# Kernel optimization log

Hardware: AMD Instinct MI355X
Metric: run time of the kernel (lower is better)

## Reference

```python
import jax, jax.numpy as jnp
import numpy as np

TEMPERATURE = 1.0
NEG = -1e9
EPS = 1e-8


def setup_inputs() -> dict:
    key = jax.random.key(0)
    k1, k2, k3 = jax.random.split(key, 3)
    B, H = 524288, 32
    scores = jax.random.normal(k1, (B, H), dtype=jnp.float32)
    rankings = jax.random.randint(k2, (B, H), 0, 33, dtype=jnp.int32)
    mask = jax.random.randint(k3, (B, H), 0, 2, dtype=jnp.int32).astype(bool)
    return {"scores": scores, "rankings": rankings, "mask": mask}


def reference(scores, rankings, mask):
    B, H = scores.shape
    # effective validity: horse present AND has a ranking > 0 (top_k=None)
    m = mask & (rankings > 0)
    # masked, temperature-scaled scores; -1e9 entries underflow to exactly 0 in softmax
    s = jnp.where(m, scores / TEMPERATURE, NEG)
    p = jax.nn.softmax(s, axis=1)  # [B, H], ~0 at invalid slots

    n_valid = jnp.sum(m, axis=1)  # [B]
    # ideal order: valid horses sorted by ranking ascending (invalid pushed to end)
    rank_key = jnp.where(m, rankings, jnp.iinfo(jnp.int32).max)
    rank_order = jnp.argsort(rank_key, axis=1)          # stable sort
    # prediction order: valid horses in original index order (matches torch.where)
    pos_order = jnp.argsort(~m, axis=1)                 # stable: valid first

    q = jnp.take_along_axis(p, rank_order, axis=1)      # ideal_probs, aligned by list position
    pr = jnp.take_along_axis(p, pos_order, axis=1)      # pred_probs,  aligned by list position

    # positions >= n_valid are padding
    valid_pos = jnp.arange(H)[None, :] < n_valid[:, None]
    q_safe = jnp.where(valid_pos, q, 1.0)
    pr_safe = jnp.where(valid_pos, pr, 1.0)
    # KL(ideal || pred) with the original's log(pred + 1e-8)
    kl_terms = q_safe * (jnp.log(q_safe) - jnp.log(pr_safe + EPS))
    kl = jnp.sum(jnp.where(valid_pos, kl_terms, 0.0), axis=1)  # [B]

    # rows with <= 1 valid ranked horse are skipped entirely
    row_ok = n_valid > 1
    n_rows = jnp.maximum(jnp.sum(row_ok), 1)
    return jnp.sum(jnp.where(row_ok, kl, 0.0)) / n_rows  # reduction='mean'
```

## Files before the change

kernel.cpp:

```cpp
#include <hip/hip_runtime.h>
#include <stdint.h>


#define H 32
#define BLK 256
#define WPB 4
#define ROWD 17
#define WREGION (64 * ROWD)

__global__ __launch_bounds__(BLK) void listwise_kernel(
    const float* __restrict__ scores,
    const int* __restrict__ rankings,
    const unsigned char* __restrict__ mask_u8,
    float* __restrict__ part_kl,
    float* __restrict__ part_cnt,
    int nrows)
{
    __shared__ uint32_t stage[WPB * WREGION];
    __shared__ float s_kl[WPB], s_cnt[WPB];

    const int tid  = threadIdx.x;
    const int lane = tid & 63;
    const int wid  = tid >> 6;
    uint32_t* wbuf = &stage[wid * WREGION];
    const int wrow0 = blockIdx.x * BLK + wid * 64;

    float kl = 0.0f, cnt = 0.0f;
    uint32_t kp[16], sw[16];
    int nv = 0;
    bool have_row = false;
    unsigned short* rowp = (unsigned short*)&wbuf[lane * ROWD];

    const bool full = (wrow0 + 64 <= nrows);

    uint4 pr[8], ps[8];
    uint32_t pmw[8];
    if (full) {
        const uint4* r4 = (const uint4*)(rankings + (size_t)wrow0 * H);
        const uint4* s4 = (const uint4*)(scores + (size_t)wrow0 * H);
        const uint32_t* m1 = (const uint32_t*)(mask_u8 + (size_t)wrow0 * H);
        #pragma unroll
        for (int c = 0; c < 8; ++c) pr[c] = r4[lane + 64 * c];
        #pragma unroll
        for (int c = 0; c < 8; ++c) ps[c] = s4[lane + 64 * c];
        #pragma unroll
        for (int c = 0; c < 8; ++c) pmw[c] = m1[lane + 64 * c];
    }

    unsigned char probe = mask_u8[lane];
    const bool mask_is_i32 =
        (__ballot(((lane & 3) != 0) && (probe != 0)) == 0ull);

    if (full) {
        have_row = true;

        #pragma unroll
        for (int c = 0; c < 8; ++c) {
            const uint4 v = ps[c];
            const int L = (lane + 64 * c) << 2;
            uint32_t* d = &wbuf[(L >> 5) * ROWD + ((L & 31) >> 1)];
            d[0] = ((v.x + 0x8000u) >> 16) | (((v.y + 0x8000u) >> 16) << 16);
            d[1] = ((v.z + 0x8000u) >> 16) | (((v.w + 0x8000u) >> 16) << 16);
        }
        {
            const uint32_t* rb = &wbuf[lane * ROWD];
            #pragma unroll
            for (int a = 0; a < 16; ++a) sw[a] = rb[a];
        }

        if (!mask_is_i32) {
            #pragma unroll
            for (int c = 0; c < 8; ++c) {
                const uint4 rv = pr[c];
                const uint32_t mv = pmw[c];
                const int L = (lane + 64 * c) << 2;
                const uint32_t t0 = ((mv & 0x000000FFu) != 0u && (int)rv.x > 0) ? (rv.x << 5) : 0x4000u;
                const uint32_t t1 = ((mv & 0x0000FF00u) != 0u && (int)rv.y > 0) ? (rv.y << 5) : 0x4000u;
                const uint32_t t2 = ((mv & 0x00FF0000u) != 0u && (int)rv.z > 0) ? (rv.z << 5) : 0x4000u;
                const uint32_t t3 = ((mv & 0xFF000000u) != 0u && (int)rv.w > 0) ? (rv.w << 5) : 0x4000u;
                uint32_t* d = &wbuf[(L >> 5) * ROWD + ((L & 31) >> 1)];
                d[0] = t0 | (t1 << 16);
                d[1] = t2 | (t3 << 16);
            }
        } else {
            const uint4* m4 =
                (const uint4*)((const uint32_t*)mask_u8 + (size_t)wrow0 * H);
            #pragma unroll
            for (int c = 0; c < 8; ++c) {
                const uint4 rv = pr[c];
                const uint4 mv = m4[lane + 64 * c];
                const int L = (lane + 64 * c) << 2;
                const uint32_t t0 = (mv.x != 0u && (int)rv.x > 0) ? (rv.x << 5) : 0x4000u;
                const uint32_t t1 = (mv.y != 0u && (int)rv.y > 0) ? (rv.y << 5) : 0x4000u;
                const uint32_t t2 = (mv.z != 0u && (int)rv.z > 0) ? (rv.z << 5) : 0x4000u;
                const uint32_t t3 = (mv.w != 0u && (int)rv.w > 0) ? (rv.w << 5) : 0x4000u;
                uint32_t* d = &wbuf[(L >> 5) * ROWD + ((L & 31) >> 1)];
                d[0] = t0 | (t1 << 16);
                d[1] = t2 | (t3 << 16);
            }
        }
        {
            const uint32_t* rb = &wbuf[lane * ROWD];
            uint32_t inv2 = 0;
            #pragma unroll
            for (int a = 0; a < 16; ++a) {
                const uint32_t w = rb[a];
                kp[a] = w | ((uint32_t)(2 * a) | (((uint32_t)(2 * a + 1)) << 16));
                inv2 += (w >> 14) & 0x00010001u;
            }
            nv = 32 - (int)((inv2 & 0xFFFFu) + (inv2 >> 16));
        }
        {
            int jp = 0;
            #pragma unroll
            for (int a = 0; a < 16; ++a) {
                const uint32_t s2 = sw[a];
                const uint32_t kw = kp[a];
                const bool v0 = (kw & 0xFFFFu) < 0x4000u;
                const bool v1 = (kw >> 16) < 0x4000u;
                rowp[v0 ? jp : 33] = (unsigned short)(s2 & 0xFFFFu);
                jp += v0 ? 1 : 0;
                rowp[v1 ? jp : 33] = (unsigned short)(s2 >> 16);
                jp += v1 ? 1 : 0;
            }
        }
    } else if (wrow0 + lane < nrows) {
        have_row = true;
        const int row = wrow0 + lane;
        const int*   rptr = rankings + (size_t)row * H;
        const float* sptr = scores + (size_t)row * H;
        uint32_t vbits = 0;
        if (mask_is_i32) {
            const int* mp = (const int*)mask_u8 + (size_t)row * H;
            #pragma unroll
            for (int k = 0; k < H; ++k) vbits |= (mp[k] != 0 ? 1u : 0u) << k;
        } else {
            const unsigned char* mp = mask_u8 + (size_t)row * H;
            #pragma unroll
            for (int k = 0; k < H; ++k) vbits |= (mp[k] != 0 ? 1u : 0u) << k;
        }
        int jp = 0;
        #pragma unroll
        for (int a = 0; a < 16; ++a) {
            uint32_t kq[2], bq[2];
            #pragma unroll
            for (int q = 0; q < 2; ++q) {
                const int k = 2 * a + q;
                const int r = rptr[k];
                const bool valid = (((vbits >> k) & 1u) != 0u) && (r > 0);
                kq[q] = valid ? ((((uint32_t)r) << 5) | (uint32_t)k)
                              : (0x4000u | (uint32_t)k);
                nv += valid ? 1 : 0;
                bq[q] = (__float_as_uint(sptr[k]) + 0x8000u) >> 16;
                rowp[valid ? jp : 33] = (unsigned short)bq[q];
                jp += valid ? 1 : 0;
            }
            kp[a] = kq[0] | (kq[1] << 16);
            sw[a] = bq[0] | (bq[1] << 16);
        }
    }

    if (have_row) {
        uint32_t w32[32];
        #pragma unroll
        for (int a = 0; a < 16; ++a) {
            const uint32_t kw = kp[a], s2 = sw[a];
            w32[2 * a]     = (kw << 16) | (s2 & 0xFFFFu);
            w32[2 * a + 1] = (kw & 0xFFFF0000u) | (s2 >> 16);
        }
        #pragma unroll
        for (int k = 2; k <= 32; k <<= 1) {
            #pragma unroll
            for (int j = k >> 1; j > 0; j >>= 1) {
                #pragma unroll
                for (int i = 0; i < 32; ++i) {
                    const int l = i ^ j;
                    if (l > i) {
                        const uint32_t a = w32[i], b = w32[l];
                        const uint32_t mn = a < b ? a : b;
                        const uint32_t mx = a < b ? b : a;
                        const bool up = ((i & k) == 0);
                        w32[i] = up ? mn : mx;
                        w32[l] = up ? mx : mn;
                    }
                }
            }
        }

        float se = 0.0f, num = 0.0f;
        const uint32_t* rbd = &wbuf[lane * ROWD];
        #pragma unroll
        for (int a = 0; a < 16; ++a) {
            const uint32_t cw = rbd[a];
            #pragma unroll
            for (int q = 0; q < 2; ++q) {
                const uint32_t wv = w32[2 * a + q];
                const bool valid = wv < 0x40000000u;
                const float s_i = __uint_as_float(wv << 16);
                const uint32_t c16 = q ? (cw >> 16) : (cw & 0xFFFFu);
                const float g = __uint_as_float(c16 << 16);
                float e = __expf(s_i);
                e = valid ? e : 0.0f;
                const float d2 = valid ? (s_i - g) : 0.0f;
                se += e;
                num = __builtin_fmaf(e, d2, num);
            }
        }
        if (nv > 1) { kl = __fdividef(num, se); cnt = 1.0f; }
    }

    #pragma unroll
    for (int m = 32; m >= 1; m >>= 1) {
        kl  += __shfl_xor(kl, m);
        cnt += __shfl_xor(cnt, m);
    }
    if (lane == 0) { s_kl[wid] = kl; s_cnt[wid] = cnt; }
    __syncthreads();
    if (tid == 0) {
        part_kl[blockIdx.x]  = s_kl[0] + s_kl[1] + s_kl[2] + s_kl[3];
        part_cnt[blockIdx.x] = s_cnt[0] + s_cnt[1] + s_cnt[2] + s_cnt[3];
    }
}

__global__ __launch_bounds__(256) void finalize_kernel(
    const float* __restrict__ part_kl,
    const float* __restrict__ part_cnt,
    float* __restrict__ out, int nblk)
{
    float k = 0.0f, c = 0.0f;
    for (int i = threadIdx.x; i < nblk; i += 256) {
        k += part_kl[i];
        c += part_cnt[i];
    }
    #pragma unroll
    for (int m = 32; m >= 1; m >>= 1) {
        k += __shfl_xor(k, m);
        c += __shfl_xor(c, m);
    }
    __shared__ float sk[4], sc[4];
    const int wid = threadIdx.x >> 6;
    if ((threadIdx.x & 63) == 0) { sk[wid] = k; sc[wid] = c; }
    __syncthreads();
    if (threadIdx.x == 0) {
        float K = sk[0] + sk[1] + sk[2] + sk[3];
        float C = sc[0] + sc[1] + sc[2] + sc[3];
        if (C < 1.0f) C = 1.0f;
        out[0] = K / C;
    }
}

extern "C" void kernel_launch(void* const* d_in, const int* in_sizes, int n_in,
                              void* d_out, int out_size, void* d_ws, size_t ws_size,
                              hipStream_t stream) {
    const float* scores = (const float*)d_in[0];
    const int* rankings = (const int*)d_in[1];
    const unsigned char* mask = (const unsigned char*)d_in[2];
    float* out = (float*)d_out;

    const int total = in_sizes[0];
    const int nrows = total / H;
    const int blocks = (nrows + BLK - 1) / BLK;

    float* part_kl  = (float*)d_ws;
    float* part_cnt = (float*)d_ws + blocks;

    listwise_kernel<<<blocks, BLK, 0, stream>>>(
        scores, rankings, mask, part_kl, part_cnt, nrows);

    finalize_kernel<<<1, 256, 0, stream>>>(part_kl, part_cnt, out, blocks);
}
```

Measured before the change: 199.7 us.

## Replace LDS compaction with second bitonic sort for prediction order

Rather than compacting valid scores through LDS with scattered 16-bit stores, the kernel builds a second key array (validity and column index packed with the score) and sorts it with a bitonic network in registers, which yields the prediction order. The staging layout changes to one packed 32-bit word per element, written with uint4 stores and row stride 36. n_valid>1 is now tested on the second sorted element. This removes the serial compaction pass and scattered LDS traffic but doubles the sorting ALU work and raises register pressure, with a launch-bounds hint of 4.

```diff
diff --git a/kernel.cpp b/kernel.cpp
--- a/kernel.cpp
+++ b/kernel.cpp
@@ -5,10 +5,31 @@
 #define H 32
 #define BLK 256
 #define WPB 4
-#define ROWD 17
+#define ROWD 36
 #define WREGION (64 * ROWD)
 
-__global__ __launch_bounds__(BLK) void listwise_kernel(
+__device__ __forceinline__ void sort32(uint32_t* w) {
+    #pragma unroll
+    for (int k = 2; k <= 32; k <<= 1) {
+        #pragma unroll
+        for (int j = k >> 1; j > 0; j >>= 1) {
+            #pragma unroll
+            for (int i = 0; i < 32; ++i) {
+                const int l = i ^ j;
+                if (l > i) {
+                    const uint32_t a = w[i], b = w[l];
+                    const uint32_t mn = a < b ? a : b;
+                    const uint32_t mx = a < b ? b : a;
+                    const bool up = ((i & k) == 0);
+                    w[i] = up ? mn : mx;
+                    w[l] = up ? mx : mn;
+                }
+            }
+        }
+    }
+}
+
+__global__ __launch_bounds__(BLK, 4) void listwise_kernel(
     const float* __restrict__ scores,
     const int* __restrict__ rankings,
     const unsigned char* __restrict__ mask_u8,
@@ -16,7 +37,7 @@
     float* __restrict__ part_cnt,
     int nrows)
 {
-    __shared__ uint32_t stage[WPB * WREGION];
+    __shared__ __align__(16) uint32_t stage[WPB * WREGION];
     __shared__ float s_kl[WPB], s_cnt[WPB];
 
     const int tid  = threadIdx.x;
@@ -24,111 +45,110 @@
     const int wid  = tid >> 6;
     uint32_t* wbuf = &stage[wid * WREGION];
     const int wrow0 = blockIdx.x * BLK + wid * 64;
-
-    float kl = 0.0f, cnt = 0.0f;
-    uint32_t kp[16], sw[16];
-    int nv = 0;
-    bool have_row = false;
-    unsigned short* rowp = (unsigned short*)&wbuf[lane * ROWD];
-
     const bool full = (wrow0 + 64 <= nrows);
 
+    unsigned char probe = mask_u8[lane];
+
     uint4 pr[8], ps[8];
-    uint32_t pmw[8];
     if (full) {
         const uint4* r4 = (const uint4*)(rankings + (size_t)wrow0 * H);
         const uint4* s4 = (const uint4*)(scores + (size_t)wrow0 * H);
-        const uint32_t* m1 = (const uint32_t*)(mask_u8 + (size_t)wrow0 * H);
         #pragma unroll
         for (int c = 0; c < 8; ++c) pr[c] = r4[lane + 64 * c];
         #pragma unroll
         for (int c = 0; c < 8; ++c) ps[c] = s4[lane + 64 * c];
-        #pragma unroll
-        for (int c = 0; c < 8; ++c) pmw[c] = m1[lane + 64 * c];
-    }
-
-    unsigned char probe = mask_u8[lane];
+    }
     const bool mask_is_i32 =
         (__ballot(((lane & 3) != 0) && (probe != 0)) == 0ull);
 
+    float kl = 0.0f, cnt = 0.0f;
+    uint32_t w1[32], w2[32];
+    bool have_row = false;
+
     if (full) {
         have_row = true;
-
-        #pragma unroll
-        for (int c = 0; c < 8; ++c) {
-            const uint4 v = ps[c];
-            const int L = (lane + 64 * c) << 2;
-            uint32_t* d = &wbuf[(L >> 5) * ROWD + ((L & 31) >> 1)];
-            d[0] = ((v.x + 0x8000u) >> 16) | (((v.y + 0x8000u) >> 16) << 16);
-            d[1] = ((v.z + 0x8000u) >> 16) | (((v.w + 0x8000u) >> 16) << 16);
-        }
-        {
-            const uint32_t* rb = &wbuf[lane * ROWD];
-            #pragma unroll
-            for (int a = 0; a < 16; ++a) sw[a] = rb[a];
-        }
+        const uint32_t colb  = 4u * (lane & 7);
+        const int      wbase = (lane >> 3) * ROWD + (int)colb;
 
         if (!mask_is_i32) {
+            const uint32_t* m1 = (const uint32_t*)(mask_u8 + (size_t)wrow0 * H);
             #pragma unroll
             for (int c = 0; c < 8; ++c) {
-                const uint4 rv = pr[c];
-                const uint32_t mv = pmw[c];
-                const int L = (lane + 64 * c) << 2;
-                const uint32_t t0 = ((mv & 0x000000FFu) != 0u && (int)rv.x > 0) ? (rv.x << 5) : 0x4000u;
-                const uint32_t t1 = ((mv & 0x0000FF00u) != 0u && (int)rv.y > 0) ? (rv.y << 5) : 0x4000u;
-                const uint32_t t2 = ((mv & 0x00FF0000u) != 0u && (int)rv.z > 0) ? (rv.z << 5) : 0x4000u;
-                const uint32_t t3 = ((mv & 0xFF000000u) != 0u && (int)rv.w > 0) ? (rv.w << 5) : 0x4000u;
-                uint32_t* d = &wbuf[(L >> 5) * ROWD + ((L & 31) >> 1)];
-                d[0] = t0 | (t1 << 16);
-                d[1] = t2 | (t3 << 16);
+                const uint32_t mv = m1[lane + 64 * c];
+                const uint4 rv = pr[c], sv = ps[c];
+                uint4 t;
+                {
+                    const bool v = ((mv & 0x000000FFu) != 0u) && ((int)rv.x > 0);
+                    const uint32_t key = v ? ((rv.x << 5) | colb) : (0x4000u | colb);
+                    t.x = (key << 16) | ((sv.x + 0x8000u) >> 16);
+                }
+                {
+                    const bool v = ((mv & 0x0000FF00u) != 0u) && ((int)rv.y > 0);
+                    const uint32_t key = v ? ((rv.y << 5) | (colb + 1)) : (0x4000u | (colb + 1));
+                    t.y = (key << 16) | ((sv.y + 0x8000u) >> 16);
+                }
+                {
+                    const bool v = ((mv & 0x00FF0000u) != 0u) && ((int)rv.z > 0);
+                    const uint32_t key = v ? ((rv.z << 5) | (colb + 2)) : (0x4000u | (colb + 2));
+                    t.z = (key << 16) | ((sv.z + 0x8000u) >> 16);
+                }
+                {
+                    const bool v = ((mv & 0xFF000000u) != 0u) && ((int)rv.w > 0);
+                    const uint32_t key = v ? ((rv.w << 5) | (colb + 3)) : (0x4000u | (colb + 3));
+                    t.w = (key << 16) | ((sv.w + 0x8000u) >> 16);
+                }
+                *(uint4*)&wbuf[wbase + 8 * ROWD * c] = t;
             }
         } else {
             const uint4* m4 =
                 (const uint4*)((const uint32_t*)mask_u8 + (size_t)wrow0 * H);
             #pragma unroll
             for (int c = 0; c < 8; ++c) {
-                const uint4 rv = pr[c];
                 const uint4 mv = m4[lane + 64 * c];
-                const int L = (lane + 64 * c) << 2;
-                const uint32_t t0 = (mv.x != 0u && (int)rv.x > 0) ? (rv.x << 5) : 0x4000u;
-                const uint32_t t1 = (mv.y != 0u && (int)rv.y > 0) ? (rv.y << 5) : 0x4000u;
-                const uint32_t t2 = (mv.z != 0u && (int)rv.z > 0) ? (rv.z << 5) : 0x4000u;
-                const uint32_t t3 = (mv.w != 0u && (int)rv.w > 0) ? (rv.w << 5) : 0x4000u;
-                uint32_t* d = &wbuf[(L >> 5) * ROWD + ((L & 31) >> 1)];
-                d[0] = t0 | (t1 << 16);
-                d[1] = t2 | (t3 << 16);
+                const uint4 rv = pr[c], sv = ps[c];
+                uint4 t;
+                {
+                    const bool v = (mv.x != 0u) && ((int)rv.x > 0);
+                    const uint32_t key = v ? ((rv.x << 5) | colb) : (0x4000u | colb);
+                    t.x = (key << 16) | ((sv.x + 0x8000u) >> 16);
+                }
+                {
+                    const bool v = (mv.y != 0u) && ((int)rv.y > 0);
+                    const uint32_t key = v ? ((rv.y << 5) | (colb + 1)) : (0x4000u | (colb + 1));
+                    t.y = (key << 16) | ((sv.y + 0x8000u) >> 16);
+                }
+                {
+                    const bool v = (mv.z != 0u) && ((int)rv.z > 0);
+                    const uint32_t key = v ? ((rv.z << 5) | (colb + 2)) : (0x4000u | (colb + 2));
+                    t.z = (key << 16) | ((sv.z + 0x8000u) >> 16);
+                }
+                {
+                    const bool v = (mv.w != 0u) && ((int)rv.w > 0);
+                    const uint32_t key = v ? ((rv.w << 5) | (colb + 3)) : (0x4000u | (colb + 3));
+                    t.w = (key << 16) | ((sv.w + 0x8000u) >> 16);
+                }
+                *(uint4*)&wbuf[wbase + 8 * ROWD * c] = t;
             }
         }
-        {
-            const uint32_t* rb = &wbuf[lane * ROWD];
-            uint32_t inv2 = 0;
-            #pragma unroll
-            for (int a = 0; a < 16; ++a) {
-                const uint32_t w = rb[a];
-                kp[a] = w | ((uint32_t)(2 * a) | (((uint32_t)(2 * a + 1)) << 16));
-                inv2 += (w >> 14) & 0x00010001u;
-            }
-            nv = 32 - (int)((inv2 & 0xFFFFu) + (inv2 >> 16));
-        }
-        {
-            int jp = 0;
-            #pragma unroll
-            for (int a = 0; a < 16; ++a) {
-                const uint32_t s2 = sw[a];
-                const uint32_t kw = kp[a];
-                const bool v0 = (kw & 0xFFFFu) < 0x4000u;
-                const bool v1 = (kw >> 16) < 0x4000u;
-                rowp[v0 ? jp : 33] = (unsigned short)(s2 & 0xFFFFu);
-                jp += v0 ? 1 : 0;
-                rowp[v1 ? jp : 33] = (unsigned short)(s2 >> 16);
-                jp += v1 ? 1 : 0;
-            }
+
+        #pragma unroll
+        for (int p = 0; p < 8; ++p) {
+            const uint4 v = *(const uint4*)&wbuf[lane * ROWD + 4 * p];
+            w1[4 * p]     = v.x;
+            w1[4 * p + 1] = v.y;
+            w1[4 * p + 2] = v.z;
+            w1[4 * p + 3] = v.w;
+        }
+        #pragma unroll
+        for (int i = 0; i < 32; ++i) {
+            const uint32_t w = w1[i];
+            w2[i] = (w < 0x40000000u) ? (w & 0x001FFFFFu) : w;
         }
     } else if (wrow0 + lane < nrows) {
         have_row = true;
         const int row = wrow0 + lane;
-        const int*   rptr = rankings + (size_t)row * H;
-        const float* sptr = scores + (size_t)row * H;
+        const uint2* rp2 = (const uint2*)(rankings + (size_t)row * H);
+        const uint2* sp2 = (const uint2*)(scores + (size_t)row * H);
         uint32_t vbits = 0;
         if (mask_is_i32) {
             const int* mp = (const int*)mask_u8 + (size_t)row * H;
@@ -139,74 +159,42 @@
             #pragma unroll
             for (int k = 0; k < H; ++k) vbits |= (mp[k] != 0 ? 1u : 0u) << k;
         }
-        int jp = 0;
-        #pragma unroll
-        for (int a = 0; a < 16; ++a) {
-            uint32_t kq[2], bq[2];
-            #pragma unroll
-            for (int q = 0; q < 2; ++q) {
-                const int k = 2 * a + q;
-                const int r = rptr[k];
-                const bool valid = (((vbits >> k) & 1u) != 0u) && (r > 0);
-                kq[q] = valid ? ((((uint32_t)r) << 5) | (uint32_t)k)
-                              : (0x4000u | (uint32_t)k);
-                nv += valid ? 1 : 0;
-                bq[q] = (__float_as_uint(sptr[k]) + 0x8000u) >> 16;
-                rowp[valid ? jp : 33] = (unsigned short)bq[q];
-                jp += valid ? 1 : 0;
-            }
-            kp[a] = kq[0] | (kq[1] << 16);
-            sw[a] = bq[0] | (bq[1] << 16);
+        #pragma unroll
+        for (int p = 0; p < 16; ++p) {
+            const uint2 rr = rp2[p];
+            const uint2 ss = sp2[p];
+            const uint32_t k0 = 2 * p, k1 = 2 * p + 1;
+            const uint32_t b0 = (ss.x + 0x8000u) >> 16;
+            const uint32_t b1 = (ss.y + 0x8000u) >> 16;
+            const bool v0 = ((vbits >> k0) & 1u) && ((int)rr.x > 0);
+            const bool v1 = ((vbits >> k1) & 1u) && ((int)rr.y > 0);
+            w1[2 * p]     = ((v0 ? ((rr.x << 5) | k0) : (0x4000u | k0)) << 16) | b0;
+            w1[2 * p + 1] = ((v1 ? ((rr.y << 5) | k1) : (0x4000u | k1)) << 16) | b1;
+            w2[2 * p]     = ((v0 ? k0 : (0x4000u | k0)) << 16) | b0;
+            w2[2 * p + 1] = ((v1 ? k1 : (0x4000u | k1)) << 16) | b1;
         }
     }
 
     if (have_row) {
-        uint32_t w32[32];
-        #pragma unroll
-        for (int a = 0; a < 16; ++a) {
-            const uint32_t kw = kp[a], s2 = sw[a];
-            w32[2 * a]     = (kw << 16) | (s2 & 0xFFFFu);
-            w32[2 * a + 1] = (kw & 0xFFFF0000u) | (s2 >> 16);
-        }
-        #pragma unroll
-        for (int k = 2; k <= 32; k <<= 1) {
-            #pragma unroll
-            for (int j = k >> 1; j > 0; j >>= 1) {
-                #pragma unroll
-                for (int i = 0; i < 32; ++i) {
-                    const int l = i ^ j;
-                    if (l > i) {
-                        const uint32_t a = w32[i], b = w32[l];
-                        const uint32_t mn = a < b ? a : b;
-                        const uint32_t mx = a < b ? b : a;
-                        const bool up = ((i & k) == 0);
-                        w32[i] = up ? mn : mx;
-                        w32[l] = up ? mx : mn;
-                    }
-                }
-            }
-        }
-
+        sort32(w1);
+        sort32(w2);
         float se = 0.0f, num = 0.0f;
-        const uint32_t* rbd = &wbuf[lane * ROWD];
-        #pragma unroll
-        for (int a = 0; a < 16; ++a) {
-            const uint32_t cw = rbd[a];
-            #pragma unroll
-            for (int q = 0; q < 2; ++q) {
-                const uint32_t wv = w32[2 * a + q];
-                const bool valid = wv < 0x40000000u;
-                const float s_i = __uint_as_float(wv << 16);
-                const uint32_t c16 = q ? (cw >> 16) : (cw & 0xFFFFu);
-                const float g = __uint_as_float(c16 << 16);
-                float e = __expf(s_i);
-                e = valid ? e : 0.0f;
-                const float d2 = valid ? (s_i - g) : 0.0f;
-                se += e;
-                num = __builtin_fmaf(e, d2, num);
-            }
-        }
-        if (nv > 1) { kl = __fdividef(num, se); cnt = 1.0f; }
+        #pragma unroll
+        for (int i = 0; i < 32; ++i) {
+            const uint32_t a = w1[i], c = w2[i];
+            const bool valid = a < 0x40000000u;
+            const float s_i = __uint_as_float(a << 16);
+            const float g   = __uint_as_float(c << 16);
+            float e = __expf(s_i);
+            e = valid ? e : 0.0f;
+            const float d2 = valid ? (s_i - g) : 0.0f;
+            se += e;
+            num = __builtin_fmaf(e, d2, num);
+        }
+        if (w1[1] < 0x40000000u) {
+            kl = __fdividef(num, se);
+            cnt = 1.0f;
+        }
     }
 
     #pragma unroll
```

After: 205.8 us. 3.1% more time.
